# Kernel optimization log

Measured on AMD Instinct MI355X. Metric: run time of the kernel, lower is better.

The kernel has to match this reference:

```python
import jax, jax.numpy as jnp
import numpy as np

S = 256      # batch == seq_len (required by the module's einsum index aliasing)
E = 1024     # emb_size
H = 16       # num_heads
D = E // H   # head dim
SCALE = float(np.sqrt(E))  # applied AFTER softmax, as in the original


def setup_inputs() -> dict:
    key = jax.random.key(0)
    ks = jax.random.split(key, 9)
    std = 1.0 / float(np.sqrt(E))
    lin = lambda k: jax.random.uniform(k, (E, E), jnp.float32, -std, std)
    b = lambda k: jax.random.uniform(k, (E,), jnp.float32, -std, std)
    return {
        "x": jax.random.normal(ks[0], (S, S, E), jnp.float32),
        "Wq": lin(ks[1]), "bq": b(jax.random.fold_in(ks[1], 1)),
        "Wk": lin(ks[2]), "bk": b(jax.random.fold_in(ks[2], 1)),
        "Wv": lin(ks[3]), "bv": b(jax.random.fold_in(ks[3], 1)),
        "Wp": lin(ks[4]), "bp": b(jax.random.fold_in(ks[4], 1)),
    }


def reference(x, Wq, bq, Wk, bk, Wv, bv, Wp, bp):
    # Linear projections (torch Linear: y = x @ W.T + b), split into heads.
    q = (x @ Wq.T + bq).reshape(S, S, H, D)  # (i, j, h, d)
    k = (x @ Wk.T + bk).reshape(S, S, H, D)
    v = (x @ Wv.T + bv).reshape(S, S, H, D)
    # Faithful to torch.einsum('bhqd,hbkd->bhqk', Q, K): K's leading two axes
    # are read transposed relative to Q, giving an HxH head-vs-head score map
    # per (i, j) token pair.
    energy = jnp.einsum('ijqd,jikd->ijqk', q, k)          # (S, S, H, H)
    # softmax over the QUERY-head axis (dim=2), then scale (post-softmax!)
    att = jax.nn.softmax(energy, axis=2) / SCALE
    # torch.einsum('bhal,bhlv->bhav', att, V)
    out = jnp.einsum('ijal,ijlv->ijav', att, v).reshape(S, S, E)
    return out @ Wp.T + bp
```

## Files before the change

### kernel.cpp

```cpp
#include <hip/hip_runtime.h>
#include <stdint.h>

#define KK_  1024

typedef __bf16 bf16x8 __attribute__((ext_vector_type(8)));
typedef float  f32x4  __attribute__((ext_vector_type(4)));

__device__ __forceinline__ void cp16(void* lds, const void* g) {
  __builtin_amdgcn_global_load_lds(
      (const __attribute__((address_space(1))) void*)g,
      (__attribute__((address_space(3))) void*)lds, 16, 0, 0);
}

__device__ __forceinline__ float b2f(unsigned short u) {
  union { unsigned int i; float f; } x;
  x.i = ((unsigned int)u) << 16;
  return x.f;
}

__device__ __forceinline__ unsigned short f2b(float f) {
  unsigned int u = __builtin_bit_cast(unsigned int, f);
  unsigned int lsb = (u >> 16) & 1u;
  u += 0x7fffu + lsb;
  return (unsigned short)(u >> 16);
}

__global__ __launch_bounds__(256) void cvt_f32_bf16(
    const float* __restrict__ src, unsigned short* __restrict__ dst, int n) {
  int i = (blockIdx.x * 256 + threadIdx.x) * 4;
  if (i < n) {
    float4 v = *(const float4*)(src + i);
    ushort4 r;
    r.x = f2b(v.x); r.y = f2b(v.y); r.z = f2b(v.z); r.w = f2b(v.w);
    *(ushort4*)(dst + i) = r;
  }
}

template <bool OUT_F32>
__global__ __launch_bounds__(256) void gemm_bt(
    const unsigned short* __restrict__ A,
    const unsigned short* __restrict__ W0,
    const unsigned short* __restrict__ W1,
    const unsigned short* __restrict__ W2,
    const float* __restrict__ b0,
    const float* __restrict__ b1,
    const float* __restrict__ b2,
    void* __restrict__ Cout,
    int Nout) {
  __shared__ __align__(16) unsigned short sA[128 * 64];
  __shared__ __align__(16) unsigned short sB[128 * 64];

  const int t  = threadIdx.x;
  const int bx = blockIdx.x;
  const int by = blockIdx.y;
  const int wsel = by >> 3;
  const int nloc = (by & 7) * 128;
  const unsigned short* Wm = (wsel == 0) ? W0 : ((wsel == 1) ? W1 : W2);
  const float* bias        = (wsel == 0) ? b0 : ((wsel == 1) ? b1 : b2);

  const int ar = t >> 3;
  const int ac = (t & 7) * 8;
  const unsigned short* gA = A  + (size_t)(bx * 128 + ar) * KK_ + ac;
  const unsigned short* gB = Wm + (size_t)(nloc + ar) * KK_ + ac;

  const int lane = t & 63;
  const int wv = t >> 6;
  const int wm = (wv >> 1) * 64;
  const int wn = (wv & 1) * 64;
  const int fr = lane & 15;
  const int fk = (lane >> 4) * 8;

  f32x4 zero = {0.f, 0.f, 0.f, 0.f};
  f32x4 acc[4][4];
#pragma unroll
  for (int a = 0; a < 4; ++a)
#pragma unroll
    for (int b = 0; b < 4; ++b) acc[a][b] = zero;

  for (int k0 = 0; k0 < KK_; k0 += 64) {
#pragma unroll
    for (int it = 0; it < 4; ++it) {
      cp16(sA + t * 8 + it * 2048, gA + (size_t)it * 32 * KK_ + k0);
      cp16(sB + t * 8 + it * 2048, gB + (size_t)it * 32 * KK_ + k0);
    }
    __syncthreads();

#pragma unroll
    for (int kk = 0; kk < 64; kk += 32) {
      bf16x8 af[4], bfv[4];
#pragma unroll
      for (int mt = 0; mt < 4; ++mt)
        af[mt] = *(const bf16x8*)(sA + (wm + mt * 16 + fr) * 64 + kk + fk);
#pragma unroll
      for (int nt = 0; nt < 4; ++nt)
        bfv[nt] = *(const bf16x8*)(sB + (wn + nt * 16 + fr) * 64 + kk + fk);
#pragma unroll
      for (int mt = 0; mt < 4; ++mt)
#pragma unroll
        for (int nt = 0; nt < 4; ++nt)
          acc[mt][nt] = __builtin_amdgcn_mfma_f32_16x16x32_bf16(
              af[mt], bfv[nt], acc[mt][nt], 0, 0, 0);
    }
    __syncthreads();
  }

  const int cc = lane & 15;
  const int rq = (lane >> 4) * 4;
#pragma unroll
  for (int mt = 0; mt < 4; ++mt) {
#pragma unroll
    for (int nt = 0; nt < 4; ++nt) {
      const int gn = by * 128 + wn + nt * 16 + cc;
      const float bb = bias[nloc + wn + nt * 16 + cc];
#pragma unroll
      for (int r = 0; r < 4; ++r) {
        const int gm = bx * 128 + wm + mt * 16 + rq + r;
        const float val = acc[mt][nt][r] + bb;
        if (OUT_F32)
          ((float*)Cout)[(size_t)gm * Nout + gn] = val;
        else
          ((unsigned short*)Cout)[(size_t)gm * Nout + gn] = f2b(val);
      }
    }
  }
}

__global__ __launch_bounds__(256) void attn_kernel(
    const unsigned short* __restrict__ qkv,
    unsigned short* __restrict__ ao) {
  __shared__ float sq[16 * 68];
  __shared__ float sk[16 * 68];
  __shared__ float sv[16 * 68];
  __shared__ float se[16 * 17];
  __shared__ float satt[16 * 17];
  __shared__ float smax[16];
  __shared__ float sscale[16];

  const int t = threadIdx.x;
  const int b = blockIdx.x;
  const int i = b >> 8;
  const int j = b & 255;

  const size_t rq = (size_t)b * 3072;
  const size_t rk = (size_t)(j * 256 + i) * 3072 + 1024;
  const size_t rv = rq + 2048;

  const ushort4 uq = ((const ushort4*)(qkv + rq))[t];
  const ushort4 uk = ((const ushort4*)(qkv + rk))[t];
  const ushort4 uv = ((const ushort4*)(qkv + rv))[t];

  const int h  = t >> 4;
  const int d0 = (t & 15) * 4;
  {
    float* p = sq + h * 68 + d0;
    p[0] = b2f(uq.x); p[1] = b2f(uq.y); p[2] = b2f(uq.z); p[3] = b2f(uq.w);
    p = sk + h * 68 + d0;
    p[0] = b2f(uk.x); p[1] = b2f(uk.y); p[2] = b2f(uk.z); p[3] = b2f(uk.w);
    p = sv + h * 68 + d0;
    p[0] = b2f(uv.x); p[1] = b2f(uv.y); p[2] = b2f(uv.z); p[3] = b2f(uv.w);
  }
  __syncthreads();

  const int qh = h;
  const int kh = t & 15;
  float e = 0.f;
  {
    const float4* qr = (const float4*)(sq + qh * 68);
    const float4* kr = (const float4*)(sk + kh * 68);
#pragma unroll
    for (int c = 0; c < 16; ++c) {
      const float4 a = qr[c];
      const float4 bb = kr[c];
      e += a.x * bb.x + a.y * bb.y + a.z * bb.z + a.w * bb.w;
    }
  }
  se[qh * 17 + kh] = e;
  __syncthreads();

  if (t < 16) {
    float m = -1e30f;
#pragma unroll
    for (int q = 0; q < 16; ++q) m = fmaxf(m, se[q * 17 + t]);
    float s = 0.f;
#pragma unroll
    for (int q = 0; q < 16; ++q) s += __expf(se[q * 17 + t] - m);
    smax[t] = m;
    sscale[t] = 1.0f / (32.0f * s);
  }
  __syncthreads();
  satt[qh * 17 + kh] = __expf(e - smax[kh]) * sscale[kh];
  __syncthreads();

  float o0 = 0.f, o1 = 0.f, o2 = 0.f, o3 = 0.f;
#pragma unroll
  for (int l = 0; l < 16; ++l) {
    const float w = satt[qh * 17 + l];
    const float4 vv = *(const float4*)(sv + l * 68 + d0);
    o0 += w * vv.x; o1 += w * vv.y; o2 += w * vv.z; o3 += w * vv.w;
  }
  ushort4 r;
  r.x = f2b(o0); r.y = f2b(o1); r.z = f2b(o2); r.w = f2b(o3);
  ((ushort4*)(ao + (size_t)b * 1024))[t] = r;
}

extern "C" void kernel_launch(void* const* d_in, const int* in_sizes, int n_in,
                              void* d_out, int out_size, void* d_ws, size_t ws_size,
                              hipStream_t stream) {
  const float* x  = (const float*)d_in[0];
  const float* Wq = (const float*)d_in[1];
  const float* bq = (const float*)d_in[2];
  const float* Wk = (const float*)d_in[3];
  const float* bk = (const float*)d_in[4];
  const float* Wv = (const float*)d_in[5];
  const float* bv = (const float*)d_in[6];
  const float* Wp = (const float*)d_in[7];
  const float* bp = (const float*)d_in[8];
  float* out = (float*)d_out;

  unsigned short* qkv     = (unsigned short*)d_ws;
  unsigned short* ao      = qkv + (size_t)65536 * 3072;
  unsigned short* Wqkv_bf = ao  + (size_t)65536 * 1024;
  unsigned short* Wp_bf   = Wqkv_bf + (size_t)3072 * 1024;
  unsigned short* x_bf = (unsigned short*)d_out;

  const int NX = 65536 * 1024;
  const int NW = 1024 * 1024;

  cvt_f32_bf16<<<NX / 1024, 256, 0, stream>>>(x, x_bf, NX);
  cvt_f32_bf16<<<NW / 1024, 256, 0, stream>>>(Wq, Wqkv_bf, NW);
  cvt_f32_bf16<<<NW / 1024, 256, 0, stream>>>(Wk, Wqkv_bf + (size_t)NW, NW);
  cvt_f32_bf16<<<NW / 1024, 256, 0, stream>>>(Wv, Wqkv_bf + (size_t)2 * NW, NW);
  cvt_f32_bf16<<<NW / 1024, 256, 0, stream>>>(Wp, Wp_bf, NW);

  gemm_bt<false><<<dim3(512, 24), dim3(256), 0, stream>>>(
      x_bf, Wqkv_bf, Wqkv_bf + (size_t)NW, Wqkv_bf + (size_t)2 * NW,
      bq, bk, bv, (void*)qkv, 3072);
  attn_kernel<<<dim3(65536), dim3(256), 0, stream>>>(qkv, ao);
  gemm_bt<true><<<dim3(512, 8), dim3(256), 0, stream>>>(
      ao, Wp_bf, Wp_bf, Wp_bf, bp, bp, bp, (void*)out, 1024);
}
```

Baseline: 1.473 ms.

## Swizzle GEMM LDS tiles and rewrite attention as one-wave MFMA per token pair

The GEMM's LDS layout is XOR-swizzled on both the global-to-LDS copy and the fragment reads, to remove bank conflicts when lanes read bf16x8 fragments. The attention kernel now gives each (i,j) pair to a single wavefront instead of a 256-thread block. The head-by-head score map is computed with two MFMA instructions, the softmax over query heads uses cross-lane shuffles, and the V accumulation reads bf16 straight from global memory. This drops the LDS staging and the many __syncthreads per pair, but V is reread per lane group and the shuffle-based indexing must map heads correctly.

```diff
diff --git a/kernel.cpp b/kernel.cpp
--- a/kernel.cpp
+++ b/kernel.cpp
@@ -5,6 +5,7 @@
 
 typedef __bf16 bf16x8 __attribute__((ext_vector_type(8)));
 typedef float  f32x4  __attribute__((ext_vector_type(4)));
+typedef unsigned short u16x8 __attribute__((ext_vector_type(8)));
 
 __device__ __forceinline__ void cp16(void* lds, const void* g) {
   __builtin_amdgcn_global_load_lds(
@@ -59,7 +60,7 @@
   const float* bias        = (wsel == 0) ? b0 : ((wsel == 1) ? b1 : b2);
 
   const int ar = t >> 3;
-  const int ac = (t & 7) * 8;
+  const int ac = ((t & 7) * 8) ^ ((ar & 7) * 8);
   const unsigned short* gA = A  + (size_t)(bx * 128 + ar) * KK_ + ac;
   const unsigned short* gB = Wm + (size_t)(nloc + ar) * KK_ + ac;
 
@@ -69,6 +70,7 @@
   const int wn = (wv & 1) * 64;
   const int fr = lane & 15;
   const int fk = (lane >> 4) * 8;
+  const int swz = (fr & 7) << 4;
 
   f32x4 zero = {0.f, 0.f, 0.f, 0.f};
   f32x4 acc[4][4];
@@ -90,10 +92,12 @@
       bf16x8 af[4], bfv[4];
 #pragma unroll
       for (int mt = 0; mt < 4; ++mt)
-        af[mt] = *(const bf16x8*)(sA + (wm + mt * 16 + fr) * 64 + kk + fk);
+        af[mt] = *(const bf16x8*)((const unsigned char*)sA +
+            ((((wm + mt * 16 + fr) * 64 + kk + fk) * 2) ^ swz));
 #pragma unroll
       for (int nt = 0; nt < 4; ++nt)
-        bfv[nt] = *(const bf16x8*)(sB + (wn + nt * 16 + fr) * 64 + kk + fk);
+        bfv[nt] = *(const bf16x8*)((const unsigned char*)sB +
+            ((((wn + nt * 16 + fr) * 64 + kk + fk) * 2) ^ swz));
 #pragma unroll
       for (int mt = 0; mt < 4; ++mt)
 #pragma unroll
@@ -125,82 +129,69 @@
   }
 }
 
-__global__ __launch_bounds__(256) void attn_kernel(
+__global__ __launch_bounds__(256) void attn_wave(
     const unsigned short* __restrict__ qkv,
     unsigned short* __restrict__ ao) {
-  __shared__ float sq[16 * 68];
-  __shared__ float sk[16 * 68];
-  __shared__ float sv[16 * 68];
-  __shared__ float se[16 * 17];
-  __shared__ float satt[16 * 17];
-  __shared__ float smax[16];
-  __shared__ float sscale[16];
-
-  const int t = threadIdx.x;
-  const int b = blockIdx.x;
-  const int i = b >> 8;
-  const int j = b & 255;
-
-  const size_t rq = (size_t)b * 3072;
-  const size_t rk = (size_t)(j * 256 + i) * 3072 + 1024;
-  const size_t rv = rq + 2048;
-
-  const ushort4 uq = ((const ushort4*)(qkv + rq))[t];
-  const ushort4 uk = ((const ushort4*)(qkv + rk))[t];
-  const ushort4 uv = ((const ushort4*)(qkv + rv))[t];
-
-  const int h  = t >> 4;
-  const int d0 = (t & 15) * 4;
-  {
-    float* p = sq + h * 68 + d0;
-    p[0] = b2f(uq.x); p[1] = b2f(uq.y); p[2] = b2f(uq.z); p[3] = b2f(uq.w);
-    p = sk + h * 68 + d0;
-    p[0] = b2f(uk.x); p[1] = b2f(uk.y); p[2] = b2f(uk.z); p[3] = b2f(uk.w);
-    p = sv + h * 68 + d0;
-    p[0] = b2f(uv.x); p[1] = b2f(uv.y); p[2] = b2f(uv.z); p[3] = b2f(uv.w);
-  }
-  __syncthreads();
-
-  const int qh = h;
-  const int kh = t & 15;
-  float e = 0.f;
-  {
-    const float4* qr = (const float4*)(sq + qh * 68);
-    const float4* kr = (const float4*)(sk + kh * 68);
-#pragma unroll
-    for (int c = 0; c < 16; ++c) {
-      const float4 a = qr[c];
-      const float4 bb = kr[c];
-      e += a.x * bb.x + a.y * bb.y + a.z * bb.z + a.w * bb.w;
-    }
-  }
-  se[qh * 17 + kh] = e;
-  __syncthreads();
-
-  if (t < 16) {
-    float m = -1e30f;
-#pragma unroll
-    for (int q = 0; q < 16; ++q) m = fmaxf(m, se[q * 17 + t]);
-    float s = 0.f;
-#pragma unroll
-    for (int q = 0; q < 16; ++q) s += __expf(se[q * 17 + t] - m);
-    smax[t] = m;
-    sscale[t] = 1.0f / (32.0f * s);
-  }
-  __syncthreads();
-  satt[qh * 17 + kh] = __expf(e - smax[kh]) * sscale[kh];
-  __syncthreads();
-
-  float o0 = 0.f, o1 = 0.f, o2 = 0.f, o3 = 0.f;
-#pragma unroll
-  for (int l = 0; l < 16; ++l) {
-    const float w = satt[qh * 17 + l];
-    const float4 vv = *(const float4*)(sv + l * 68 + d0);
-    o0 += w * vv.x; o1 += w * vv.y; o2 += w * vv.z; o3 += w * vv.w;
-  }
-  ushort4 r;
-  r.x = f2b(o0); r.y = f2b(o1); r.z = f2b(o2); r.w = f2b(o3);
-  ((ushort4*)(ao + (size_t)b * 1024))[t] = r;
+  const int lane = threadIdx.x & 63;
+  const int p = blockIdx.x * 4 + (threadIdx.x >> 6);
+  const int i = p >> 8;
+  const int j = p & 255;
+
+  const unsigned short* q = qkv + (size_t)p * 3072;
+  const unsigned short* k = qkv + (size_t)(j * 256 + i) * 3072 + 1024;
+  const unsigned short* v = q + 2048;
+
+  const int fr = lane & 15;
+  const int g  = lane >> 4;
+  const int fk = g * 8;
+
+  const bf16x8 kf0 = *(const bf16x8*)(k + fr * 64 + fk);
+  const bf16x8 kf1 = *(const bf16x8*)(k + fr * 64 + 32 + fk);
+  const bf16x8 qf0 = *(const bf16x8*)(q + fr * 64 + fk);
+  const bf16x8 qf1 = *(const bf16x8*)(q + fr * 64 + 32 + fk);
+
+  f32x4 e = {0.f, 0.f, 0.f, 0.f};
+  e = __builtin_amdgcn_mfma_f32_16x16x32_bf16(kf0, qf0, e, 0, 0, 0);
+  e = __builtin_amdgcn_mfma_f32_16x16x32_bf16(kf1, qf1, e, 0, 0, 0);
+
+  float att[4];
+#pragma unroll
+  for (int r = 0; r < 4; ++r) {
+    float m = e[r];
+#pragma unroll
+    for (int mask = 1; mask <= 8; mask <<= 1)
+      m = fmaxf(m, __shfl_xor(m, mask));
+    const float pe = __expf(e[r] - m);
+    float s = pe;
+#pragma unroll
+    for (int mask = 1; mask <= 8; mask <<= 1)
+      s += __shfl_xor(s, mask);
+    att[r] = pe / (32.0f * s);
+  }
+
+  const int c0 = g * 16;
+  float o[16];
+#pragma unroll
+  for (int u = 0; u < 16; ++u) o[u] = 0.f;
+
+#pragma unroll
+  for (int kh = 0; kh < 16; ++kh) {
+    const float w = __shfl(att[kh & 3], fr + (kh >> 2) * 16);
+    const u16x8 v0 = *(const u16x8*)(v + kh * 64 + c0);
+    const u16x8 v1 = *(const u16x8*)(v + kh * 64 + c0 + 8);
+#pragma unroll
+    for (int u = 0; u < 8; ++u) {
+      o[u]     += w * b2f(v0[u]);
+      o[8 + u] += w * b2f(v1[u]);
+    }
+  }
+
+  u16x8 r0, r1;
+#pragma unroll
+  for (int u = 0; u < 8; ++u) { r0[u] = f2b(o[u]); r1[u] = f2b(o[8 + u]); }
+  unsigned short* dst = ao + (size_t)p * 1024 + fr * 64 + c0;
+  *(u16x8*)dst       = r0;
+  *(u16x8*)(dst + 8) = r1;
 }
 
 extern "C" void kernel_launch(void* const* d_in, const int* in_sizes, int n_in,
@@ -235,7 +226,7 @@
   gemm_bt<false><<<dim3(512, 24), dim3(256), 0, stream>>>(
       x_bf, Wqkv_bf, Wqkv_bf + (size_t)NW, Wqkv_bf + (size_t)2 * NW,
       bq, bk, bv, (void*)qkv, 3072);
-  attn_kernel<<<dim3(65536), dim3(256), 0, stream>>>(qkv, ao);
+  attn_wave<<<dim3(65536 / 4), dim3(256), 0, stream>>>(qkv, ao);
   gemm_bt<true><<<dim3(512, 8), dim3(256), 0, stream>>>(
       ao, Wp_bf, Wp_bf, Wp_bf, bp, bp, bp, (void*)out, 1024);
 }
```

Result: faster. 1.410 ms (-4.3%).
